# Optimization experiments

Hardware: AMD Instinct MI355X
Metric: run time of the kernel (lower is better)

Reference implementation:

```python
import jax, jax.numpy as jnp
import numpy as np

B, T, C, H = 4, 2048, 1024, 16
D = C // H  # head dim = 64

def setup_inputs() -> dict:
    key = jax.random.key(0)
    k1, k2, k3 = jax.random.split(key, 3)
    y = jax.random.normal(k1, (B, T, C), dtype=jnp.float32)
    W_attn = jax.random.normal(k2, (C, 3 * C), dtype=jnp.float32) * (1.0 / np.sqrt(C))
    b_attn = jnp.zeros((3 * C,), dtype=jnp.float32)
    W_proj = jax.random.normal(k3, (C, C), dtype=jnp.float32) * (1.0 / np.sqrt(C))
    b_proj = jnp.zeros((C,), dtype=jnp.float32)
    return {"y": y, "W_attn": W_attn, "b_attn": b_attn, "W_proj": W_proj, "b_proj": b_proj}

def reference(y, W_attn, b_attn, W_proj, b_proj):
    # qkv projection: [B,T,C] @ [C,3C] -> split into q,k,v
    qkv = y @ W_attn + b_attn
    q, k, v = jnp.split(qkv, 3, axis=-1)
    # [B,T,C] -> [B,H,T,D]
    q = q.reshape(B, T, H, D).swapaxes(1, 2)
    k = k.reshape(B, T, H, D).swapaxes(1, 2)
    v = v.reshape(B, T, H, D).swapaxes(1, 2)
    # scaled dot-product attention, non-causal (config default), dropout=0
    att = jnp.einsum('bhtd,bhrd->bhtr', q, k) * (1.0 / jnp.sqrt(jnp.float32(D)))
    att = jax.nn.softmax(att, axis=-1)
    out = jnp.einsum('bhts,bhsd->bhtd', att, v)
    out = out.swapaxes(1, 2).reshape(B, T, C)
    return out @ W_proj + b_proj
```

## Files before the change

### kernel.cpp

```cpp
#include <hip/hip_runtime.h>
#include <hip/hip_bf16.h>
#include <stdint.h>

#define B_ 4
#define T_ 2048
#define C_ 1024
#define H_ 16
#define D_ 64

typedef short bf16x8 __attribute__((ext_vector_type(8)));
typedef float f32x4 __attribute__((ext_vector_type(4)));
typedef unsigned short u16;

__device__ __forceinline__ u16 f2bf(float f) {
    __hip_bfloat16 h = __float2bfloat16(f);
    return *reinterpret_cast<u16*>(&h);
}

__device__ __forceinline__ void gload16(const void* g, void* l) {
    __builtin_amdgcn_global_load_lds(
        (const __attribute__((address_space(1))) unsigned int*)g,
        (__attribute__((address_space(3))) unsigned int*)l, 16, 0, 0);
}

__global__ void k_cast_bf16(const float* __restrict__ src, u16* __restrict__ dst, int n) {
    int i = (blockIdx.x * blockDim.x + threadIdx.x) * 4;
    if (i >= n) return;
    float4 f = *reinterpret_cast<const float4*>(src + i);
    ushort4 o;
    o.x = f2bf(f.x); o.y = f2bf(f.y); o.z = f2bf(f.z); o.w = f2bf(f.w);
    *reinterpret_cast<ushort4*>(dst + i) = o;
}

__global__ void k_transpose_bf16(const float* __restrict__ src, u16* __restrict__ dst,
                                 int R, int Cc) {
    __shared__ float tile[32][33];
    int c0 = blockIdx.x * 32, r0 = blockIdx.y * 32;
    int tx = threadIdx.x, ty = threadIdx.y;
#pragma unroll
    for (int i = 0; i < 4; i++)
        tile[ty + i * 8][tx] = src[(size_t)(r0 + ty + i * 8) * Cc + c0 + tx];
    __syncthreads();
#pragma unroll
    for (int i = 0; i < 4; i++)
        dst[(size_t)(c0 + ty + i * 8) * R + r0 + tx] = f2bf(tile[tx][ty + i * 8]);
}

template <int EPI>
__launch_bounds__(256, 2)
__global__ void k_gemm(const u16* __restrict__ A, const u16* __restrict__ Bt,
                       const float* __restrict__ bias, int K, int N,
                       float* __restrict__ outf,
                       u16* __restrict__ qw, u16* __restrict__ kw, u16* __restrict__ vw) {
    __shared__ u16 As[128 * 64];
    __shared__ u16 Bs[128 * 64];
    const int tid = threadIdx.x;
    const int lane = tid & 63, w = tid >> 6;
    const int m0 = blockIdx.x * 128, n0 = blockIdx.y * 128;
    const int wm = (w >> 1) * 64, wn = (w & 1) * 64;
    const int lr = lane & 15, lg = lane >> 4;

    f32x4 acc[4][4];
#pragma unroll
    for (int i = 0; i < 4; i++)
#pragma unroll
        for (int j = 0; j < 4; j++) acc[i][j] = (f32x4){0.f, 0.f, 0.f, 0.f};

    const int nk = K >> 6;
    for (int kt = 0; kt < nk; ++kt) {
        const int k0 = kt * 64;
#pragma unroll
        for (int i = 0; i < 4; i++) {
            int c = i * 256 + tid;
            int row = c >> 3, k8 = (c & 7) << 3;
            gload16(A + (size_t)(m0 + row) * K + k0 + k8, (char*)As + i * 4096 + w * 1024);
            gload16(Bt + (size_t)(n0 + row) * K + k0 + k8, (char*)Bs + i * 4096 + w * 1024);
        }
        __syncthreads();
#pragma unroll
        for (int kk = 0; kk < 2; ++kk) {
            bf16x8 af[4], bfr[4];
#pragma unroll
            for (int mf = 0; mf < 4; ++mf)
                af[mf] = *reinterpret_cast<const bf16x8*>(&As[(wm + mf * 16 + lr) * 64 + kk * 32 + lg * 8]);
#pragma unroll
            for (int nf = 0; nf < 4; ++nf)
                bfr[nf] = *reinterpret_cast<const bf16x8*>(&Bs[(wn + nf * 16 + lr) * 64 + kk * 32 + lg * 8]);
#pragma unroll
            for (int mf = 0; mf < 4; ++mf)
#pragma unroll
                for (int nf = 0; nf < 4; ++nf)
                    acc[mf][nf] = __builtin_amdgcn_mfma_f32_16x16x32_bf16(af[mf], bfr[nf], acc[mf][nf], 0, 0, 0);
        }
        __syncthreads();
    }

    if (EPI == 0) {
#pragma unroll
        for (int mf = 0; mf < 4; ++mf)
#pragma unroll
            for (int nf = 0; nf < 4; ++nf) {
                int ng = n0 + wn + nf * 16 + lr;
                float bs = bias[ng];
#pragma unroll
                for (int r = 0; r < 4; ++r) {
                    int mg = m0 + wm + mf * 16 + lg * 4 + r;
                    outf[(size_t)mg * N + ng] = acc[mf][nf][r] + bs;
                }
            }
    } else {
        const int sec = n0 >> 10;
#pragma unroll
        for (int mf = 0; mf < 4; ++mf)
#pragma unroll
            for (int nf = 0; nf < 4; ++nf) {
                int ng = n0 + wn + nf * 16 + lr;
                float bs = bias[ng];
                int hd = ng & 1023;
                int h = hd >> 6, d = hd & 63;
                int mgb = m0 + wm + mf * 16 + lg * 4;
                int b = mgb >> 11, t0v = mgb & 2047;
                if (sec == 2) {
                    ushort4 pk;
                    pk.x = f2bf(acc[mf][nf][0] + bs);
                    pk.y = f2bf(acc[mf][nf][1] + bs);
                    pk.z = f2bf(acc[mf][nf][2] + bs);
                    pk.w = f2bf(acc[mf][nf][3] + bs);
                    *reinterpret_cast<ushort4*>(&vw[((size_t)(b * H_ + h) * D_ + d) * T_ + t0v]) = pk;
                } else {
                    u16* dst = (sec == 0) ? qw : kw;
#pragma unroll
                    for (int r = 0; r < 4; ++r)
                        dst[((size_t)(b * H_ + h) * T_ + t0v + r) * D_ + d] = f2bf(acc[mf][nf][r] + bs);
                }
            }
    }
}

__launch_bounds__(256, 3)
__global__ void k_attn(const u16* __restrict__ qw, const u16* __restrict__ kw,
                       const u16* __restrict__ vw, u16* __restrict__ attn) {
    __shared__ u16 Ks[2][64][64];
    __shared__ u16 Vs[2][64][64];
    __shared__ u16 pshm[4][32][64];
    const int tid = threadIdx.x, lane = tid & 63, w = tid >> 6;
    const int lr = lane & 15, lg = lane >> 4;
    const int bid = blockIdx.x;
    const int logical = (bid & 7) * 128 + (bid >> 3);
    const int bh = logical >> 4, qb = logical & 15;
    const int b = bh >> 4, h = bh & 15;
    const int q0 = qb * 128 + w * 32;
    const u16* qbase = qw + (size_t)bh * T_ * D_;
    const u16* kbase = kw + (size_t)bh * T_ * D_;
    const u16* vbase = vw + (size_t)bh * D_ * T_;

    bf16x8 qf[2][2];
#pragma unroll
    for (int jq = 0; jq < 2; jq++)
#pragma unroll
        for (int kd = 0; kd < 2; kd++)
            qf[jq][kd] = *reinterpret_cast<const bf16x8*>(
                &qbase[(size_t)(q0 + jq * 16 + lr) * D_ + kd * 32 + lg * 8]);

    auto stageK = [&](int kt, int buf) {
#pragma unroll
        for (int i = 0; i < 2; i++) {
            int idx = i * 256 + tid;
            int row = idx >> 3, ch = idx & 7;
            int gch = ch ^ (row & 7);
            gload16(kbase + ((size_t)(kt * 64 + row) * 64 + gch * 8),
                    (char*)&Ks[buf][0][0] + i * 4096 + w * 1024);
        }
    };
    auto stageV = [&](int kt, int buf) {
#pragma unroll
        for (int i = 0; i < 2; i++) {
            int idx = i * 256 + tid;
            int row = idx >> 3, ch = idx & 7;
            int gch = ch ^ (row & 7);
            gload16(vbase + ((size_t)row * T_ + kt * 64 + gch * 8),
                    (char*)&Vs[buf][0][0] + i * 4096 + w * 1024);
        }
    };

    f32x4 o[4][2];
#pragma unroll
    for (int md = 0; md < 4; md++)
#pragma unroll
        for (int jq = 0; jq < 2; jq++) o[md][jq] = (f32x4){0.f, 0.f, 0.f, 0.f};
    float m_run[2] = {-INFINITY, -INFINITY};
    float l_run[2] = {0.f, 0.f};

    const int NT = T_ / 64;
    stageK(0, 0);
    stageV(0, 0);

    for (int kt = 0; kt < NT; ++kt) {
        const int cur = kt & 1;
        if (kt + 1 < NT) {
            stageK(kt + 1, cur ^ 1);
            stageV(kt + 1, cur ^ 1);
            asm volatile("s_waitcnt vmcnt(4)" ::: "memory");
        } else {
            asm volatile("s_waitcnt vmcnt(0)" ::: "memory");
        }
        __builtin_amdgcn_s_barrier();

        bf16x8 ka[4][2];
#pragma unroll
        for (int mk = 0; mk < 4; mk++)
#pragma unroll
            for (int kd = 0; kd < 2; kd++) {
                int row = mk * 16 + lr;
                int colb = (kd * 64 + lg * 16) ^ ((row & 7) << 4);
                ka[mk][kd] = *reinterpret_cast<const bf16x8*>(
                    (const char*)&Ks[cur][0][0] + row * 128 + colb);
            }

        f32x4 s[4][2];
#pragma unroll
        for (int mk = 0; mk < 4; mk++)
#pragma unroll
            for (int jq = 0; jq < 2; jq++) s[mk][jq] = (f32x4){0.f, 0.f, 0.f, 0.f};
        __builtin_amdgcn_s_setprio(1);
#pragma unroll
        for (int kd = 0; kd < 2; kd++)
#pragma unroll
            for (int mk = 0; mk < 4; mk++)
#pragma unroll
                for (int jq = 0; jq < 2; jq++)
                    s[mk][jq] = __builtin_amdgcn_mfma_f32_16x16x32_bf16(ka[mk][kd], qf[jq][kd], s[mk][jq], 0, 0, 0);
        __builtin_amdgcn_s_setprio(0);

#pragma unroll
        for (int jq = 0; jq < 2; jq++) {
            float pm = -INFINITY;
#pragma unroll
            for (int mk = 0; mk < 4; mk++)
#pragma unroll
                for (int r = 0; r < 4; r++) {
                    float v = s[mk][jq][r] * 0.125f;
                    s[mk][jq][r] = v;
                    pm = fmaxf(pm, v);
                }
            pm = fmaxf(pm, __shfl_xor(pm, 16));
            pm = fmaxf(pm, __shfl_xor(pm, 32));
            float mnew = fmaxf(m_run[jq], pm);
            float corr = __expf(m_run[jq] - mnew);
            m_run[jq] = mnew;
            float psum = 0.f;
            int prow = jq * 16 + lr;
#pragma unroll
            for (int mk = 0; mk < 4; mk++) {
                ushort4 pk;
                float p0 = __expf(s[mk][jq][0] - mnew);
                float p1 = __expf(s[mk][jq][1] - mnew);
                float p2 = __expf(s[mk][jq][2] - mnew);
                float p3 = __expf(s[mk][jq][3] - mnew);
                psum += p0 + p1 + p2 + p3;
                pk.x = f2bf(p0); pk.y = f2bf(p1); pk.z = f2bf(p2); pk.w = f2bf(p3);
                int pcolb = (mk * 32 + lg * 8) ^ ((prow & 7) << 4);
                *reinterpret_cast<ushort4*>((char*)&pshm[w][0][0] + prow * 128 + pcolb) = pk;
            }
            psum += __shfl_xor(psum, 16);
            psum += __shfl_xor(psum, 32);
            l_run[jq] = l_run[jq] * corr + psum;
#pragma unroll
            for (int md = 0; md < 4; md++)
#pragma unroll
                for (int r = 0; r < 4; r++) o[md][jq][r] *= corr;
        }
        asm volatile("s_waitcnt lgkmcnt(0)" ::: "memory");

        bf16x8 pb[2][2];
#pragma unroll
        for (int jq = 0; jq < 2; jq++)
#pragma unroll
            for (int kk = 0; kk < 2; kk++) {
                int prow = jq * 16 + lr;
                int pcolb = (kk * 64 + lg * 16) ^ ((prow & 7) << 4);
                pb[jq][kk] = *reinterpret_cast<const bf16x8*>(
                    (const char*)&pshm[w][0][0] + prow * 128 + pcolb);
            }
        bf16x8 va[4][2];
#pragma unroll
        for (int md = 0; md < 4; md++)
#pragma unroll
            for (int kk = 0; kk < 2; kk++) {
                int row = md * 16 + lr;
                int colb = (kk * 64 + lg * 16) ^ ((row & 7) << 4);
                va[md][kk] = *reinterpret_cast<const bf16x8*>(
                    (const char*)&Vs[cur][0][0] + row * 128 + colb);
            }
        __builtin_amdgcn_s_setprio(1);
#pragma unroll
        for (int md = 0; md < 4; md++)
#pragma unroll
            for (int jq = 0; jq < 2; jq++)
#pragma unroll
                for (int kk = 0; kk < 2; kk++)
                    o[md][jq] = __builtin_amdgcn_mfma_f32_16x16x32_bf16(va[md][kk], pb[jq][kk], o[md][jq], 0, 0, 0);
        __builtin_amdgcn_s_setprio(0);

        __builtin_amdgcn_s_barrier();
    }

#pragma unroll
    for (int jq = 0; jq < 2; jq++) {
        float rinv = 1.f / l_run[jq];
        int q = q0 + jq * 16 + lr;
#pragma unroll
        for (int md = 0; md < 4; md++) {
            int d0 = md * 16 + lg * 4;
            ushort4 pk;
            pk.x = f2bf(o[md][jq][0] * rinv);
            pk.y = f2bf(o[md][jq][1] * rinv);
            pk.z = f2bf(o[md][jq][2] * rinv);
            pk.w = f2bf(o[md][jq][3] * rinv);
            *reinterpret_cast<ushort4*>(&attn[((size_t)(b * T_ + q)) * C_ + h * D_ + d0]) = pk;
        }
    }
}

extern "C" void kernel_launch(void* const* d_in, const int* in_sizes, int n_in,
                              void* d_out, int out_size, void* d_ws, size_t ws_size,
                              hipStream_t stream) {
    const float* y = (const float*)d_in[0];
    const float* W_attn = (const float*)d_in[1];
    const float* b_attn = (const float*)d_in[2];
    const float* W_proj = (const float*)d_in[3];
    const float* b_proj = (const float*)d_in[4];

    char* ws = (char*)d_ws;
    u16* y_bf = (u16*)(ws);
    u16* WaT  = (u16*)(ws + 16777216);
    u16* WpT  = (u16*)(ws + 16777216 + 6291456);
    u16* q_ws = (u16*)(ws + 25165824);
    u16* k_ws = (u16*)(ws + 25165824 + 16777216);
    u16* v_ws = (u16*)(ws + 25165824 + 33554432);
    u16* attn = (u16*)(ws + 25165824 + 50331648);

    k_cast_bf16<<<8192, 256, 0, stream>>>(y, y_bf, B_ * T_ * C_);
    k_transpose_bf16<<<dim3(96, 32), dim3(32, 8), 0, stream>>>(W_attn, WaT, 1024, 3072);
    k_transpose_bf16<<<dim3(32, 32), dim3(32, 8), 0, stream>>>(W_proj, WpT, 1024, 1024);
    k_gemm<1><<<dim3(64, 24), 256, 0, stream>>>(y_bf, WaT, b_attn, 1024, 3072,
                                                nullptr, q_ws, k_ws, v_ws);
    k_attn<<<1024, 256, 0, stream>>>(q_ws, k_ws, v_ws, attn);
    k_gemm<0><<<dim3(64, 8), 256, 0, stream>>>(attn, WpT, b_proj, 1024, 1024,
                                               (float*)d_out, nullptr, nullptr, nullptr);
}
```

Baseline: 231.7 us.

## Keep P in registers via 16x16x16 MFMA, fold scale into Q, lazy rescale

Folds the softmax scale and log2(e) into Q during the QKV epilogue so attention can use raw exp2 without a per-element multiply. Skips the running-max rescale of O and l unless the max grows by more than 8 for some lane. When the 16x16x16 bf16 MFMA builtin exists, P stays in registers as that instruction's B operand instead of a round trip through LDS, and the freed LDS allows a higher occupancy hint (4 blocks per SIMD). This relies on the accumulator layout of the 16x16x32 MFMA matching the operand layout of the K=16 MFMA, and on fp32 headroom for skipped rescales.

```diff
diff --git a/kernel.cpp b/kernel.cpp
--- a/kernel.cpp
+++ b/kernel.cpp
@@ -9,12 +9,23 @@
 #define D_ 64
 
 typedef short bf16x8 __attribute__((ext_vector_type(8)));
+typedef short bf16x4 __attribute__((ext_vector_type(4)));
 typedef float f32x4 __attribute__((ext_vector_type(4)));
 typedef unsigned short u16;
+
+#define HAS_M16 __has_builtin(__builtin_amdgcn_mfma_f32_16x16x16bf16_1k)
+
+#define QSCALE 0.18033688011112042f
 
 __device__ __forceinline__ u16 f2bf(float f) {
     __hip_bfloat16 h = __float2bfloat16(f);
     return *reinterpret_cast<u16*>(&h);
+}
+
+__device__ __forceinline__ float fexp2(float x) {
+    float r;
+    asm("v_exp_f32 %0, %1" : "=v"(r) : "v"(x));
+    return r;
 }
 
 __device__ __forceinline__ void gload16(const void* g, void* l) {
@@ -110,6 +121,7 @@
             }
     } else {
         const int sec = n0 >> 10;
+        const float sc = (sec == 0) ? QSCALE : 1.0f;
 #pragma unroll
         for (int mf = 0; mf < 4; ++mf)
 #pragma unroll
@@ -131,18 +143,24 @@
                     u16* dst = (sec == 0) ? qw : kw;
 #pragma unroll
                     for (int r = 0; r < 4; ++r)
-                        dst[((size_t)(b * H_ + h) * T_ + t0v + r) * D_ + d] = f2bf(acc[mf][nf][r] + bs);
+                        dst[((size_t)(b * H_ + h) * T_ + t0v + r) * D_ + d] = f2bf((acc[mf][nf][r] + bs) * sc);
                 }
             }
     }
 }
 
+#if HAS_M16
+__launch_bounds__(256, 4)
+#else
 __launch_bounds__(256, 3)
+#endif
 __global__ void k_attn(const u16* __restrict__ qw, const u16* __restrict__ kw,
                        const u16* __restrict__ vw, u16* __restrict__ attn) {
     __shared__ u16 Ks[2][64][64];
     __shared__ u16 Vs[2][64][64];
+#if !HAS_M16
     __shared__ u16 pshm[4][32][64];
+#endif
     const int tid = threadIdx.x, lane = tid & 63, w = tid >> 6;
     const int lr = lane & 15, lg = lane >> 4;
     const int bid = blockIdx.x;
@@ -232,46 +250,70 @@
                     s[mk][jq] = __builtin_amdgcn_mfma_f32_16x16x32_bf16(ka[mk][kd], qf[jq][kd], s[mk][jq], 0, 0, 0);
         __builtin_amdgcn_s_setprio(0);
 
+#if HAS_M16
+        bf16x4 pfrag[2][4];
+#endif
 #pragma unroll
         for (int jq = 0; jq < 2; jq++) {
             float pm = -INFINITY;
 #pragma unroll
             for (int mk = 0; mk < 4; mk++)
 #pragma unroll
-                for (int r = 0; r < 4; r++) {
-                    float v = s[mk][jq][r] * 0.125f;
-                    s[mk][jq][r] = v;
-                    pm = fmaxf(pm, v);
-                }
+                for (int r = 0; r < 4; r++) pm = fmaxf(pm, s[mk][jq][r]);
             pm = fmaxf(pm, __shfl_xor(pm, 16));
             pm = fmaxf(pm, __shfl_xor(pm, 32));
-            float mnew = fmaxf(m_run[jq], pm);
-            float corr = __expf(m_run[jq] - mnew);
-            m_run[jq] = mnew;
+            if (!__all(pm - m_run[jq] <= 8.0f)) {
+                float mnew = fmaxf(m_run[jq], pm);
+                float corr = fexp2(m_run[jq] - mnew);
+                m_run[jq] = mnew;
+                l_run[jq] *= corr;
+#pragma unroll
+                for (int md = 0; md < 4; md++)
+#pragma unroll
+                    for (int r = 0; r < 4; r++) o[md][jq][r] *= corr;
+            }
+            float mcur = m_run[jq];
             float psum = 0.f;
-            int prow = jq * 16 + lr;
 #pragma unroll
             for (int mk = 0; mk < 4; mk++) {
+                float p0 = fexp2(s[mk][jq][0] - mcur);
+                float p1 = fexp2(s[mk][jq][1] - mcur);
+                float p2 = fexp2(s[mk][jq][2] - mcur);
+                float p3 = fexp2(s[mk][jq][3] - mcur);
+                psum += (p0 + p1) + (p2 + p3);
+#if HAS_M16
+                pfrag[jq][mk] = (bf16x4){(short)f2bf(p0), (short)f2bf(p1),
+                                         (short)f2bf(p2), (short)f2bf(p3)};
+#else
                 ushort4 pk;
-                float p0 = __expf(s[mk][jq][0] - mnew);
-                float p1 = __expf(s[mk][jq][1] - mnew);
-                float p2 = __expf(s[mk][jq][2] - mnew);
-                float p3 = __expf(s[mk][jq][3] - mnew);
-                psum += p0 + p1 + p2 + p3;
                 pk.x = f2bf(p0); pk.y = f2bf(p1); pk.z = f2bf(p2); pk.w = f2bf(p3);
+                int prow = jq * 16 + lr;
                 int pcolb = (mk * 32 + lg * 8) ^ ((prow & 7) << 4);
                 *reinterpret_cast<ushort4*>((char*)&pshm[w][0][0] + prow * 128 + pcolb) = pk;
+#endif
             }
             psum += __shfl_xor(psum, 16);
             psum += __shfl_xor(psum, 32);
-            l_run[jq] = l_run[jq] * corr + psum;
-#pragma unroll
-            for (int md = 0; md < 4; md++)
-#pragma unroll
-                for (int r = 0; r < 4; r++) o[md][jq][r] *= corr;
-        }
+            l_run[jq] += psum;
+        }
+
+#if HAS_M16
+        __builtin_amdgcn_s_setprio(1);
+#pragma unroll
+        for (int md = 0; md < 4; md++) {
+            int row = md * 16 + lr;
+#pragma unroll
+            for (int mk = 0; mk < 4; mk++) {
+                int colb = (mk * 32 + lg * 8) ^ ((row & 7) << 4);
+                bf16x4 va = *reinterpret_cast<const bf16x4*>(
+                    (const char*)&Vs[cur][0][0] + row * 128 + colb);
+                o[md][0] = __builtin_amdgcn_mfma_f32_16x16x16bf16_1k(va, pfrag[0][mk], o[md][0], 0, 0, 0);
+                o[md][1] = __builtin_amdgcn_mfma_f32_16x16x16bf16_1k(va, pfrag[1][mk], o[md][1], 0, 0, 0);
+            }
+        }
+        __builtin_amdgcn_s_setprio(0);
+#else
         asm volatile("s_waitcnt lgkmcnt(0)" ::: "memory");
-
         bf16x8 pb[2][2];
 #pragma unroll
         for (int jq = 0; jq < 2; jq++)
@@ -301,6 +343,7 @@
                 for (int kk = 0; kk < 2; kk++)
                     o[md][jq] = __builtin_amdgcn_mfma_f32_16x16x32_bf16(va[md][kk], pb[jq][kk], o[md][jq], 0, 0, 0);
         __builtin_amdgcn_s_setprio(0);
+#endif
 
         __builtin_amdgcn_s_barrier();
     }
```

Result: faster. 225.6 us (-2.6%).
